# Kernel tuning notes

Hardware: AMD Instinct MI355X
Metric: run time of the kernel (lower is better)

Reference implementation:

```python
import jax, jax.numpy as jnp
import numpy as np

N, D = 16384, 256

def setup_inputs() -> dict:
    key = jax.random.key(0)
    k1, k2, k3 = jax.random.split(key, 3)
    X = jax.random.normal(k1, (N, D), dtype=jnp.float32)
    W = jax.random.normal(k2, (D, D), dtype=jnp.float32) * (1.0 / np.sqrt(D))
    b = jax.random.normal(k3, (D,), dtype=jnp.float32) * (1.0 / np.sqrt(D))
    return {"X": X, "W": W, "b": b}

def reference(X, W, b):
    # Step 1: bilinear attention A = X W X^T   (N, N) -- materialized as in original
    A = (X @ W) @ X.T
    # Step 2: context aggregation Z = A X      (N, D)
    Z = A @ X
    # Step 3: output head g = Z b              (N,)
    g = Z @ b
    return g
```

## Files before the change

kernel.cpp:

```cpp
#include <hip/hip_runtime.h>

#define NROWS 16384
#define DDIM  256
#define K1BLK 512


__global__ __launch_bounds__(256) void k1_partial_v(const float* __restrict__ X,
                                                    const float* __restrict__ b,
                                                    float* __restrict__ partials) {
    const int tid  = threadIdx.x;
    const int lane = tid & 63;
    const int wave = tid >> 6;
    const int bid  = blockIdx.x;

    const float4* X4 = (const float4*)X;
    const float4  bf = ((const float4*)b)[lane];

    float4 vacc = make_float4(0.f, 0.f, 0.f, 0.f);
    const int row0 = bid * 32 + wave * 8;
    #pragma unroll
    for (int i = 0; i < 8; ++i) {
        const float4 x = X4[(row0 + i) * 64 + lane];
        float t = x.x * bf.x + x.y * bf.y + x.z * bf.z + x.w * bf.w;
        #pragma unroll
        for (int off = 32; off; off >>= 1) t += __shfl_xor(t, off, 64);
        vacc.x += t * x.x; vacc.y += t * x.y;
        vacc.z += t * x.z; vacc.w += t * x.w;
    }

    __shared__ float sp[4][DDIM];
    ((float4*)sp[wave])[lane] = vacc;
    __syncthreads();
    partials[bid * DDIM + tid] = sp[0][tid] + sp[1][tid] + sp[2][tid] + sp[3][tid];
}

__global__ __launch_bounds__(256) void k2_w2(const float* __restrict__ partials,
                                             const float* __restrict__ W,
                                             float* __restrict__ w2) {
    const int tid  = threadIdx.x;
    const int lane = tid & 63;
    const int wave = tid >> 6;

    const float4* P4 = (const float4*)partials;
    float4 acc = make_float4(0.f, 0.f, 0.f, 0.f);
    const int r0 = wave * (K1BLK / 4);
    #pragma unroll 8
    for (int j = 0; j < K1BLK / 4; ++j) {
        const float4 p = P4[(r0 + j) * 64 + lane];
        acc.x += p.x; acc.y += p.y; acc.z += p.z; acc.w += p.w;
    }

    __shared__ float4 sp4[4][64];
    sp4[wave][lane] = acc;
    __syncthreads();

    const float* spf = (const float*)sp4;
    __shared__ __align__(16) float sv[DDIM];
    sv[tid] = spf[tid] + spf[256 + tid] + spf[512 + tid] + spf[768 + tid];
    __syncthreads();

    const float4 vf = ((const float4*)sv)[lane];
    const int row = blockIdx.x * 4 + wave;
    const float4 w = ((const float4*)W)[row * 64 + lane];
    float t = w.x * vf.x + w.y * vf.y + w.z * vf.z + w.w * vf.w;
    #pragma unroll
    for (int off = 32; off; off >>= 1) t += __shfl_xor(t, off, 64);
    if (lane == 0) w2[row] = t;
}

__global__ __launch_bounds__(256) void k3_g(const float* __restrict__ X,
                                            const float* __restrict__ w2,
                                            float* __restrict__ g) {
    const int tid  = threadIdx.x;
    const int lane = tid & 63;
    const int wave = tid >> 6;

    const float4* X4 = (const float4*)X;
    const float4  wf = ((const float4*)w2)[lane];

    const int row0 = blockIdx.x * 16 + wave * 4;
    #pragma unroll
    for (int i = 0; i < 4; ++i) {
        const float4 x = X4[(row0 + i) * 64 + lane];
        float t = x.x * wf.x + x.y * wf.y + x.z * wf.z + x.w * wf.w;
        #pragma unroll
        for (int off = 32; off; off >>= 1) t += __shfl_xor(t, off, 64);
        if (lane == 0) g[row0 + i] = t;
    }
}

extern "C" void kernel_launch(void* const* d_in, const int* in_sizes, int n_in,
                              void* d_out, int out_size, void* d_ws, size_t ws_size,
                              hipStream_t stream) {
    const float* X = (const float*)d_in[0];
    const float* W = (const float*)d_in[1];
    const float* b = (const float*)d_in[2];
    float* out = (float*)d_out;

    float* partials = (float*)d_ws;
    float* w2       = partials + K1BLK * DDIM;

    k1_partial_v<<<K1BLK, 256, 0, stream>>>(X, b, partials);
    k2_w2<<<64, 256, 0, stream>>>(partials, W, w2);
    k3_g<<<1024, 256, 0, stream>>>(X, w2, out);
}
```

Measured before the change: 77.56 us.

## Reduce k1 partials via atomics into 64 slots, doubling k1 grid

The first kernel now runs 1024 blocks of 16 rows each, and each block atomically adds its partial vector into one of 64 slot rows instead of writing a per-block partials row. The second kernel therefore sums only 64 rows rather than 512, which cuts its serial read loop. In exchange, a memset launch is added to zero the slots, atomics contend on each slot, and the floating-point summation order becomes nondeterministic.

```diff
diff --git a/kernel.cpp b/kernel.cpp
--- a/kernel.cpp
+++ b/kernel.cpp
@@ -2,12 +2,13 @@
 
 #define NROWS 16384
 #define DDIM  256
-#define K1BLK 512
+#define K1BLK 1024
+#define NSLOT 64
 
 
-__global__ __launch_bounds__(256) void k1_partial_v(const float* __restrict__ X,
-                                                    const float* __restrict__ b,
-                                                    float* __restrict__ partials) {
+__global__ __launch_bounds__(256) void k1_v(const float* __restrict__ X,
+                                            const float* __restrict__ b,
+                                            float* __restrict__ slots) {
     const int tid  = threadIdx.x;
     const int lane = tid & 63;
     const int wave = tid >> 6;
@@ -17,9 +18,9 @@
     const float4  bf = ((const float4*)b)[lane];
 
     float4 vacc = make_float4(0.f, 0.f, 0.f, 0.f);
-    const int row0 = bid * 32 + wave * 8;
+    const int row0 = bid * 16 + wave * 4;
     #pragma unroll
-    for (int i = 0; i < 8; ++i) {
+    for (int i = 0; i < 4; ++i) {
         const float4 x = X4[(row0 + i) * 64 + lane];
         float t = x.x * bf.x + x.y * bf.y + x.z * bf.z + x.w * bf.w;
         #pragma unroll
@@ -31,22 +32,23 @@
     __shared__ float sp[4][DDIM];
     ((float4*)sp[wave])[lane] = vacc;
     __syncthreads();
-    partials[bid * DDIM + tid] = sp[0][tid] + sp[1][tid] + sp[2][tid] + sp[3][tid];
+    const float s = sp[0][tid] + sp[1][tid] + sp[2][tid] + sp[3][tid];
+    atomicAdd(&slots[(bid & (NSLOT - 1)) * DDIM + tid], s);
 }
 
-__global__ __launch_bounds__(256) void k2_w2(const float* __restrict__ partials,
+__global__ __launch_bounds__(256) void k2_w2(const float* __restrict__ slots,
                                              const float* __restrict__ W,
                                              float* __restrict__ w2) {
     const int tid  = threadIdx.x;
     const int lane = tid & 63;
     const int wave = tid >> 6;
 
-    const float4* P4 = (const float4*)partials;
+    const float4* S4 = (const float4*)slots;
     float4 acc = make_float4(0.f, 0.f, 0.f, 0.f);
-    const int r0 = wave * (K1BLK / 4);
-    #pragma unroll 8
-    for (int j = 0; j < K1BLK / 4; ++j) {
-        const float4 p = P4[(r0 + j) * 64 + lane];
+    const int r0 = wave * (NSLOT / 4);
+    #pragma unroll
+    for (int j = 0; j < NSLOT / 4; ++j) {
+        const float4 p = S4[(r0 + j) * 64 + lane];
         acc.x += p.x; acc.y += p.y; acc.z += p.z; acc.w += p.w;
     }
 
@@ -97,10 +99,11 @@
     const float* b = (const float*)d_in[2];
     float* out = (float*)d_out;
 
-    float* partials = (float*)d_ws;
-    float* w2       = partials + K1BLK * DDIM;
+    float* slots = (float*)d_ws;
+    float* w2    = slots + NSLOT * DDIM;
 
-    k1_partial_v<<<K1BLK, 256, 0, stream>>>(X, b, partials);
-    k2_w2<<<64, 256, 0, stream>>>(partials, W, w2);
-    k3_g<<<1024, 256, 0, stream>>>(X, w2, out);
+    hipMemsetAsync(slots, 0, NSLOT * DDIM * sizeof(float), stream);
+    k1_v <<<K1BLK, 256, 0, stream>>>(X, b, slots);
+    k2_w2<<<NSLOT, 256, 0, stream>>>(slots, W, w2);
+    k3_g <<<1024, 256, 0, stream>>>(X, w2, out);
 }
```

Measured after the change: 73.41 us. 5.3% less time.
